# Kernel optimization log

Measured on AMD Instinct MI355X. Metric: run time of the kernel, lower is better.

## Reference

```python
import jax, jax.numpy as jnp
import numpy as np

S = 64.0
M = 0.5
EPS = 1e-07
NORM_EPS = 1e-12  # matches torch F.normalize default eps
B, D, C = 512, 512, 64000


def _l2_normalize(a, axis=-1):
    n = jnp.sqrt(jnp.sum(a * a, axis=axis, keepdims=True))
    return a / jnp.maximum(n, NORM_EPS)


def setup_inputs() -> dict:
    key = jax.random.key(0)
    kx, ky, kw = jax.random.split(key, 3)
    x = jax.random.normal(kx, (B, D), dtype=jnp.float32)
    y = jax.random.randint(ky, (B,), 0, C, dtype=jnp.int64)
    # kaiming_uniform-ish init: bound = sqrt(6 / fan_in)
    bound = np.sqrt(6.0 / D).astype(np.float32)
    W = jax.random.uniform(kw, (C, D), dtype=jnp.float32, minval=-bound, maxval=bound)
    return {"x": x, "y": y, "W": W}


def reference(x, y, W):
    # cosine similarities: [B, C]
    theta = _l2_normalize(x) @ _l2_normalize(W).T
    # target logit per row
    tgt = jnp.take_along_axis(theta, y[:, None], axis=1)[:, 0]  # [B]
    numerator = S * jnp.cos(jnp.arccos(jnp.clip(tgt, -1.0 + EPS, 1.0 - EPS)) + M)
    # sum of exp(s*theta) over non-target classes (mask out target column)
    is_tgt = jnp.arange(C, dtype=y.dtype)[None, :] == y[:, None]  # [B, C]
    excl_sum = jnp.sum(jnp.where(is_tgt, 0.0, jnp.exp(S * theta)), axis=1)  # [B]
    denominator = jnp.exp(numerator) + excl_sum
    return -jnp.mean(numerator - jnp.log(denominator))
```

## Files before the change

### kernel.cpp

```cpp
#include <hip/hip_runtime.h>


#define B_N 512
#define D_N 512
#define C_N 64000
#define S_SCALE 64.0f
#define MARGIN 0.5f
#define EPS_C 1e-7f
#define NREP 16

typedef unsigned short ushort_t;
typedef __attribute__((ext_vector_type(8))) short short8;
typedef __attribute__((ext_vector_type(4))) float floatx4;
typedef __attribute__((ext_vector_type(4))) float fvec4;

__device__ __forceinline__ ushort_t f2bf(float f) {
    unsigned int u = __float_as_uint(f);
    u += 0x7fffu + ((u >> 16) & 1u);
    return (ushort_t)(u >> 16);
}

__global__ void xprep_kernel(const float* __restrict__ x,
                             ushort_t* __restrict__ xnT,
                             float* __restrict__ rowsumR) {
    int b = blockIdx.x;
    int t = threadIdx.x;
    if (b == 128) {
#pragma unroll
        for (int i = 0; i < NREP * B_N / 256; ++i)
            rowsumR[i * 256 + t] = 0.0f;
        return;
    }
    int row  = b * 4 + (t >> 6);
    int lane = t & 63;
    const float4* p = (const float4*)(x + (size_t)row * D_N);
    float4 v0 = p[lane * 2];
    float4 v1 = p[lane * 2 + 1];
    float ss = v0.x*v0.x + v0.y*v0.y + v0.z*v0.z + v0.w*v0.w
             + v1.x*v1.x + v1.y*v1.y + v1.z*v1.z + v1.w*v1.w;
#pragma unroll
    for (int off = 32; off > 0; off >>= 1) ss += __shfl_xor(ss, off);
    float sc = 1.0f / fmaxf(sqrtf(ss), 1e-12f);
    uint4 o;
    o.x = (unsigned)f2bf(v0.x*sc) | ((unsigned)f2bf(v0.y*sc) << 16);
    o.y = (unsigned)f2bf(v0.z*sc) | ((unsigned)f2bf(v0.w*sc) << 16);
    o.z = (unsigned)f2bf(v1.x*sc) | ((unsigned)f2bf(v1.y*sc) << 16);
    o.w = (unsigned)f2bf(v1.z*sc) | ((unsigned)f2bf(v1.w*sc) << 16);
    *((uint4*)(xnT + ((size_t)(lane << 9) + row) * 8)) = o;
}

__global__ __launch_bounds__(512, 4)
void gemm_fused_kernel(const float* __restrict__ W,
                       const ushort_t* __restrict__ xnT,
                       const int* __restrict__ y,
                       float* __restrict__ rowsumR,
                       float* __restrict__ tgt) {
    __shared__ ushort_t sW[64 * 512];

    int t    = threadIdx.x;
    int lane = t & 63;
    int w    = t >> 6;
    int lq   = lane >> 4;
    int lc   = lane & 15;
    int cn0  = blockIdx.x * 64;

#pragma unroll
    for (int rr = 0; rr < 8; ++rr) {
        int row = w * 8 + rr;
        const fvec4* p = (const fvec4*)(W + (size_t)(cn0 + row) * D_N);
        fvec4 a = __builtin_nontemporal_load(p + lane * 2);
        fvec4 b = __builtin_nontemporal_load(p + lane * 2 + 1);
        float ss = a.x*a.x + a.y*a.y + a.z*a.z + a.w*a.w
                 + b.x*b.x + b.y*b.y + b.z*b.z + b.w*b.w;
#pragma unroll
        for (int off = 32; off > 0; off >>= 1) ss += __shfl_xor(ss, off);
        float sc = 1.0f / fmaxf(sqrtf(ss), 1e-12f);
        uint4 o;
        o.x = (unsigned)f2bf(a.x*sc) | ((unsigned)f2bf(a.y*sc) << 16);
        o.y = (unsigned)f2bf(a.z*sc) | ((unsigned)f2bf(a.w*sc) << 16);
        o.z = (unsigned)f2bf(b.x*sc) | ((unsigned)f2bf(b.y*sc) << 16);
        o.w = (unsigned)f2bf(b.z*sc) | ((unsigned)f2bf(b.w*sc) << 16);
        int kc = lane;
        int rs = row ^ (kc & 7);
        *((uint4*)(sW + kc * 512 + rs * 8)) = o;
    }
    __syncthreads();

    floatx4 acc[4][4];
#pragma unroll
    for (int i = 0; i < 4; i++)
#pragma unroll
        for (int j = 0; j < 4; j++) acc[i][j] = (floatx4){0.f, 0.f, 0.f, 0.f};

    const ushort_t* apT[4];
#pragma unroll
    for (int tm = 0; tm < 4; tm++)
        apT[tm] = xnT + ((size_t)lq * 512 + w * 64 + tm * 16 + lc) * 8;

    short8 af[4];
#pragma unroll
    for (int tm = 0; tm < 4; tm++) af[tm] = *(const short8*)(apT[tm]);

    for (int k = 0; k < 16; ++k) {
        short8 afn[4];
        if (k < 15) {
#pragma unroll
            for (int tm = 0; tm < 4; tm++)
                afn[tm] = *(const short8*)(apT[tm] + (k + 1) * 16384);
        }
        int kc = k * 4 + lq;
        short8 bfr[4];
#pragma unroll
        for (int tn = 0; tn < 4; tn++) {
            int rs = (tn * 16 + lc) ^ (kc & 7);
            bfr[tn] = *(const short8*)(sW + kc * 512 + rs * 8);
        }
#pragma unroll
        for (int tm = 0; tm < 4; tm++)
#pragma unroll
            for (int tn = 0; tn < 4; tn++)
                acc[tm][tn] = __builtin_amdgcn_mfma_f32_16x16x32_bf16(
                    af[tm], bfr[tn], acc[tm][tn], 0, 0, 0);
        if (k < 15) {
#pragma unroll
            for (int tm = 0; tm < 4; tm++) af[tm] = afn[tm];
        }
    }

    __syncthreads();
    float* rowacc = (float*)sW;
#pragma unroll
    for (int tm = 0; tm < 4; tm++) {
#pragma unroll
        for (int r = 0; r < 4; r++) {
            int lrow = w * 64 + tm * 16 + lq * 4 + r;
            int yv   = y[lrow];
            float esum = 0.0f;
#pragma unroll
            for (int tn = 0; tn < 4; tn++) {
                int gcol = cn0 + tn * 16 + lc;
                float theta = acc[tm][tn][r];
                if (gcol == yv) {
                    tgt[lrow] = theta;
                } else {
                    esum += __expf(S_SCALE * theta);
                }
            }
#pragma unroll
            for (int off = 1; off < 16; off <<= 1) esum += __shfl_xor(esum, off);
            if (lc == 0) rowacc[lrow] = esum;
        }
    }
    __syncthreads();
    atomicAdd(&rowsumR[(blockIdx.x & (NREP - 1)) * B_N + t], rowacc[t]);
}

__global__ void finalize_kernel(const float* __restrict__ rowsumR,
                                const float* __restrict__ tgt,
                                float* __restrict__ out) {
    __shared__ float red[256];
    int t = threadIdx.x;
    float s = 0.0f;
    for (int r = t; r < B_N; r += 256) {
        float rs = 0.0f;
#pragma unroll
        for (int i = 0; i < NREP; ++i) rs += rowsumR[i * B_N + r];
        float tv = tgt[r];
        tv = fminf(fmaxf(tv, -1.0f + EPS_C), 1.0f - EPS_C);
        float num = S_SCALE * cosf(acosf(tv) + MARGIN);
        float den = expf(num) + rs;
        s += num - logf(den);
    }
    red[t] = s;
    __syncthreads();
    for (int o = 128; o > 0; o >>= 1) {
        if (t < o) red[t] += red[t + o];
        __syncthreads();
    }
    if (t == 0) out[0] = -red[0] / (float)B_N;
}

extern "C" void kernel_launch(void* const* d_in, const int* in_sizes, int n_in,
                              void* d_out, int out_size, void* d_ws, size_t ws_size,
                              hipStream_t stream) {
    const float* x = (const float*)d_in[0];
    const int*   y = (const int*)d_in[1];
    const float* W = (const float*)d_in[2];
    float* out = (float*)d_out;

    char* ws = (char*)d_ws;
    ushort_t* xnT   = (ushort_t*)ws;
    float* rowsumR  = (float*)(ws + 524288);
    float* tgt      = rowsumR + NREP * B_N;

    xprep_kernel<<<129, 256, 0, stream>>>(x, xnT, rowsumR);
    gemm_fused_kernel<<<C_N / 64, 512, 0, stream>>>(W, xnT, y, rowsumR, tgt);
    finalize_kernel<<<1, 256, 0, stream>>>(rowsumR, tgt, out);
}
```

Baseline: 220.8 us.

## Stream W tiles via global_load_lds double buffering and defer column normalization

Rather than loading and normalizing the whole 64x512 W tile up front, the GEMM kernel streams W in K-slices of 32 floats with global_load_lds into a double-buffered LDS area. Each slice is converted to unnormalized bf16 and its sum of squares is accumulated, while MFMAs run on the previous slice. The column norms are applied to the accumulators at the end. This is meant to overlap the W fetch with compute and shrink LDS use. In exchange it adds a __syncthreads per K-step, and bf16 rounding now happens before scaling, which slightly changes numerics.

```diff
diff --git a/kernel.cpp b/kernel.cpp
--- a/kernel.cpp
+++ b/kernel.cpp
@@ -12,7 +12,6 @@
 typedef unsigned short ushort_t;
 typedef __attribute__((ext_vector_type(8))) short short8;
 typedef __attribute__((ext_vector_type(4))) float floatx4;
-typedef __attribute__((ext_vector_type(4))) float fvec4;
 
 __device__ __forceinline__ ushort_t f2bf(float f) {
     unsigned int u = __float_as_uint(f);
@@ -49,13 +48,23 @@
     *((uint4*)(xnT + ((size_t)(lane << 9) + row) * 8)) = o;
 }
 
+__device__ __forceinline__ void g2ldsF(const float* g, float* l) {
+    __builtin_amdgcn_global_load_lds(
+        (const __attribute__((address_space(1))) void*)g,
+        (__attribute__((address_space(3))) void*)l, 16, 0, 0);
+}
+
 __global__ __launch_bounds__(512, 4)
 void gemm_fused_kernel(const float* __restrict__ W,
                        const ushort_t* __restrict__ xnT,
                        const int* __restrict__ y,
                        float* __restrict__ rowsumR,
                        float* __restrict__ tgt) {
-    __shared__ ushort_t sW[64 * 512];
+    __shared__ float    bufF[2][2048];
+    __shared__ ushort_t bufB[2][2048];
+    __shared__ float    red[512];
+    __shared__ float    rnormS[64];
+    __shared__ float    rowacc[512];
 
     int t    = threadIdx.x;
     int lane = t & 63;
@@ -63,72 +72,78 @@
     int lq   = lane >> 4;
     int lc   = lane & 15;
     int cn0  = blockIdx.x * 64;
-
-#pragma unroll
-    for (int rr = 0; rr < 8; ++rr) {
-        int row = w * 8 + rr;
-        const fvec4* p = (const fvec4*)(W + (size_t)(cn0 + row) * D_N);
-        fvec4 a = __builtin_nontemporal_load(p + lane * 2);
-        fvec4 b = __builtin_nontemporal_load(p + lane * 2 + 1);
-        float ss = a.x*a.x + a.y*a.y + a.z*a.z + a.w*a.w
-                 + b.x*b.x + b.y*b.y + b.z*b.z + b.w*b.w;
-#pragma unroll
-        for (int off = 32; off > 0; off >>= 1) ss += __shfl_xor(ss, off);
-        float sc = 1.0f / fmaxf(sqrtf(ss), 1e-12f);
-        uint4 o;
-        o.x = (unsigned)f2bf(a.x*sc) | ((unsigned)f2bf(a.y*sc) << 16);
-        o.y = (unsigned)f2bf(a.z*sc) | ((unsigned)f2bf(a.w*sc) << 16);
-        o.z = (unsigned)f2bf(b.x*sc) | ((unsigned)f2bf(b.y*sc) << 16);
-        o.w = (unsigned)f2bf(b.z*sc) | ((unsigned)f2bf(b.w*sc) << 16);
-        int kc = lane;
-        int rs = row ^ (kc & 7);
-        *((uint4*)(sW + kc * 512 + rs * 8)) = o;
-    }
-    __syncthreads();
-
-    floatx4 acc[4][4];
-#pragma unroll
-    for (int i = 0; i < 4; i++)
-#pragma unroll
-        for (int j = 0; j < 4; j++) acc[i][j] = (floatx4){0.f, 0.f, 0.f, 0.f};
+    int col  = t >> 3;
+    int kseg = t & 7;
+
+    const float* gW = W + (size_t)(cn0 + col) * D_N + kseg * 4;
 
     const ushort_t* apT[4];
 #pragma unroll
     for (int tm = 0; tm < 4; tm++)
         apT[tm] = xnT + ((size_t)lq * 512 + w * 64 + tm * 16 + lc) * 8;
 
+    g2ldsF(gW, &bufF[0][t * 4]);
     short8 af[4];
 #pragma unroll
     for (int tm = 0; tm < 4; tm++) af[tm] = *(const short8*)(apT[tm]);
 
-    for (int k = 0; k < 16; ++k) {
+    floatx4 acc[4][4];
+#pragma unroll
+    for (int i = 0; i < 4; i++)
+#pragma unroll
+        for (int j = 0; j < 4; j++) acc[i][j] = (floatx4){0.f, 0.f, 0.f, 0.f};
+    float ssq = 0.0f;
+
+    __syncthreads();
+
+    for (int ks = 0; ks < 16; ++ks) {
+        int cur = ks & 1;
+        if (ks < 15) g2ldsF(gW + (ks + 1) * 32, &bufF[cur ^ 1][t * 4]);
+
+        float4 wv = *(const float4*)&bufF[cur][t * 4];
+        ssq += wv.x*wv.x + wv.y*wv.y + wv.z*wv.z + wv.w*wv.w;
+        uint2 pk;
+        pk.x = (unsigned)f2bf(wv.x) | ((unsigned)f2bf(wv.y) << 16);
+        pk.y = (unsigned)f2bf(wv.z) | ((unsigned)f2bf(wv.w) << 16);
+        *(uint2*)&bufB[cur][((kseg >> 1) * 64 + col) * 8 + (kseg & 1) * 4] = pk;
+
         short8 afn[4];
-        if (k < 15) {
+        if (ks < 15) {
 #pragma unroll
             for (int tm = 0; tm < 4; tm++)
-                afn[tm] = *(const short8*)(apT[tm] + (k + 1) * 16384);
+                afn[tm] = *(const short8*)(apT[tm] + (ks + 1) * 16384);
         }
-        int kc = k * 4 + lq;
+        __syncthreads();
+
         short8 bfr[4];
 #pragma unroll
-        for (int tn = 0; tn < 4; tn++) {
-            int rs = (tn * 16 + lc) ^ (kc & 7);
-            bfr[tn] = *(const short8*)(sW + kc * 512 + rs * 8);
-        }
+        for (int tn = 0; tn < 4; tn++)
+            bfr[tn] = *(const short8*)&bufB[cur][(lq * 64 + tn * 16 + lc) * 8];
 #pragma unroll
         for (int tm = 0; tm < 4; tm++)
 #pragma unroll
             for (int tn = 0; tn < 4; tn++)
                 acc[tm][tn] = __builtin_amdgcn_mfma_f32_16x16x32_bf16(
                     af[tm], bfr[tn], acc[tm][tn], 0, 0, 0);
-        if (k < 15) {
+        if (ks < 15) {
 #pragma unroll
             for (int tm = 0; tm < 4; tm++) af[tm] = afn[tm];
         }
     }
 
-    __syncthreads();
-    float* rowacc = (float*)sW;
+    red[t] = ssq;
+    __syncthreads();
+    if (t < 64) {
+        float s = 0.0f;
+#pragma unroll
+        for (int j = 0; j < 8; j++) s += red[t * 8 + j];
+        rnormS[t] = 1.0f / fmaxf(sqrtf(s), 1e-12f);
+    }
+    __syncthreads();
+
+    float rn[4];
+#pragma unroll
+    for (int tn = 0; tn < 4; tn++) rn[tn] = rnormS[tn * 16 + lc];
 #pragma unroll
     for (int tm = 0; tm < 4; tm++) {
 #pragma unroll
@@ -139,7 +154,7 @@
 #pragma unroll
             for (int tn = 0; tn < 4; tn++) {
                 int gcol = cn0 + tn * 16 + lc;
-                float theta = acc[tm][tn][r];
+                float theta = acc[tm][tn][r] * rn[tn];
                 if (gcol == yv) {
                     tgt[lrow] = theta;
                 } else {
```

Result: slower. 270.7 us (+22.6%).
